# Optimization experiments

Hardware: AMD Instinct MI355X
Metric: run time of the kernel (lower is better)

The kernel has to match this reference:

```python
import jax, jax.numpy as jnp
import numpy as np

B, S, H, L, NH, DH, FF = 64, 128, 768, 6, 12, 64, 3072
VOCAB, MAXPOS, INTENT, TAGS = 30522, 512, 22, 122
LN_EPS = 1e-12
INV_SQRT_DH = float(1.0 / np.sqrt(DH))


def _ln(x, s, b):
    m = x.mean(-1, keepdims=True)
    v = ((x - m) ** 2).mean(-1, keepdims=True)
    return (x - m) * jax.lax.rsqrt(v + LN_EPS) * s + b


def setup_inputs():
    key = jax.random.key(0)
    cnt = [0]
    def nk():
        cnt[0] += 1
        return jax.random.fold_in(key, cnt[0])
    def nrm(shape):
        return (0.02 * jax.random.normal(nk(), shape)).astype(jnp.float32)
    inp = {
        'input_ids': jax.random.randint(nk(), (B, S), 0, VOCAB),
        'attention_mask': jnp.ones((B, S), jnp.int32),
        'intent_target': jax.random.randint(nk(), (B,), 0, INTENT),
        'slots_target': jax.random.randint(nk(), (B, S), 0, TAGS),
        'slots_mask': jnp.ones((B, S), jnp.int32),
        'word_emb': nrm((VOCAB, H)), 'pos_emb': nrm((MAXPOS, H)),
        'emb_ln_s': jnp.ones((H,)), 'emb_ln_b': jnp.zeros((H,)),
        'Wq': nrm((L, H, H)), 'bq': jnp.zeros((L, H)),
        'Wk': nrm((L, H, H)), 'bk': jnp.zeros((L, H)),
        'Wv': nrm((L, H, H)), 'bv': jnp.zeros((L, H)),
        'Wo': nrm((L, H, H)), 'bo': jnp.zeros((L, H)),
        'sa_ln_s': jnp.ones((L, H)), 'sa_ln_b': jnp.zeros((L, H)),
        'W1f': nrm((L, H, FF)), 'b1f': jnp.zeros((L, FF)),
        'W2f': nrm((L, FF, H)), 'b2f': jnp.zeros((L, H)),
        'out_ln_s': jnp.ones((L, H)), 'out_ln_b': jnp.zeros((L, H)),
        'iW1': nrm((H, 64)), 'ib1': jnp.zeros((64,)),
        'iW2': nrm((64, INTENT)), 'ib2': jnp.zeros((INTENT,)),
        'sW1': nrm((H, 256)), 'sb1': jnp.zeros((256,)),
        'sW2': nrm((256, TAGS)), 'sb2': jnp.zeros((TAGS,)),
        'crf_start': nrm((TAGS,)), 'crf_end': nrm((TAGS,)), 'crf_trans': nrm((TAGS, TAGS)),
        'log_vars': jnp.zeros((2,)),
    }
    return inp


def _encoder(input_ids, attention_mask, word_emb, pos_emb, emb_ln_s, emb_ln_b,
             Wq, bq, Wk, bk, Wv, bv, Wo, bo, sa_ln_s, sa_ln_b,
             W1f, b1f, W2f, b2f, out_ln_s, out_ln_b):
    x = word_emb[input_ids] + pos_emb[jnp.arange(S)][None]
    x = _ln(x, emb_ln_s, emb_ln_b)
    neg = jnp.where(attention_mask[:, None, None, :] > 0, 0.0, -1e9).astype(x.dtype)
    for i in range(L):
        q = (x @ Wq[i] + bq[i]).reshape(B, S, NH, DH).transpose(0, 2, 1, 3)
        k = (x @ Wk[i] + bk[i]).reshape(B, S, NH, DH).transpose(0, 2, 1, 3)
        v = (x @ Wv[i] + bv[i]).reshape(B, S, NH, DH).transpose(0, 2, 1, 3)
        scores = jnp.einsum('bhqd,bhkd->bhqk', q, k) * INV_SQRT_DH + neg
        attn = jax.nn.softmax(scores, -1)
        ctx = jnp.einsum('bhqk,bhkd->bhqd', attn, v).transpose(0, 2, 1, 3).reshape(B, S, H)
        x = _ln(x + ctx @ Wo[i] + bo[i], sa_ln_s[i], sa_ln_b[i])
        h = jax.nn.gelu(x @ W1f[i] + b1f[i], approximate=False) @ W2f[i] + b2f[i]
        x = _ln(x + h, out_ln_s[i], out_ln_b[i])
    return x


def _crf_llh(emis, tags, mask, crf_start, crf_end, crf_trans):
    # pytorch-crf log-likelihood, reduction='sum'. emis [B,S,T], mask bool [B,S]
    fmask = mask.astype(emis.dtype)
    emit_sc = jnp.take_along_axis(emis, tags[..., None], -1)[..., 0]          # [B,S]
    trans_sc = crf_trans[tags[:, :-1], tags[:, 1:]]                            # [B,S-1]
    last_idx = mask.sum(1) - 1
    last_tag = tags[jnp.arange(B), last_idx]
    num = (crf_start[tags[:, 0]] + emit_sc[:, 0]
           + ((trans_sc + emit_sc[:, 1:]) * fmask[:, 1:]).sum(1)
           + crf_end[last_tag])
    def fstep(alpha, xs):
        emit_t, m_t = xs
        nxt = jax.nn.logsumexp(alpha[:, :, None] + crf_trans[None] + emit_t[:, None, :], axis=1)
        return jnp.where(m_t[:, None], nxt, alpha), None
    alpha0 = crf_start[None] + emis[:, 0]
    alpha, _ = jax.lax.scan(fstep, alpha0, (emis[:, 1:].transpose(1, 0, 2), mask[:, 1:].T))
    denom = jax.nn.logsumexp(alpha + crf_end[None], -1)
    return jnp.sum(num - denom)


def _viterbi(emis, mask, crf_start, crf_end, crf_trans):
    ident = jnp.arange(TAGS)[None, :]
    def vstep(alpha, xs):
        emit_t, m_t = xs
        score = alpha[:, :, None] + crf_trans[None] + emit_t[:, None, :]      # [B,T,T]
        bp = jnp.where(m_t[:, None], jnp.argmax(score, 1), ident)
        alpha = jnp.where(m_t[:, None], jnp.max(score, 1), alpha)
        return alpha, bp
    alpha0 = crf_start[None] + emis[:, 0]
    alpha, bps = jax.lax.scan(vstep, alpha0, (emis[:, 1:].transpose(1, 0, 2), mask[:, 1:].T))
    last = jnp.argmax(alpha + crf_end[None], -1)                               # [B]
    def bstep(tag, bp):
        prev = jnp.take_along_axis(bp, tag[:, None], 1)[:, 0]
        return prev, prev
    _, prevs = jax.lax.scan(bstep, last, bps, reverse=True)                    # [S-1,B]
    return jnp.concatenate([prevs, last[None]], 0).T                           # [B,S]


def reference(input_ids, attention_mask, intent_target, slots_target, slots_mask,
              word_emb, pos_emb, emb_ln_s, emb_ln_b,
              Wq, bq, Wk, bk, Wv, bv, Wo, bo, sa_ln_s, sa_ln_b,
              W1f, b1f, W2f, b2f, out_ln_s, out_ln_b,
              iW1, ib1, iW2, ib2, sW1, sb1, sW2, sb2,
              crf_start, crf_end, crf_trans, log_vars):
    x = _encoder(input_ids, attention_mask, word_emb, pos_emb, emb_ln_s, emb_ln_b,
                 Wq, bq, Wk, bk, Wv, bv, Wo, bo, sa_ln_s, sa_ln_b,
                 W1f, b1f, W2f, b2f, out_ln_s, out_ln_b)
    # intent head: linear1(relu(cls)) -> relu -> linear2 (dropout = eval identity)
    intent_logits = jax.nn.relu(jax.nn.relu(x[:, 0]) @ iW1 + ib1) @ iW2 + ib2
    intent_loss = (jax.nn.logsumexp(intent_logits, -1)
                   - jnp.take_along_axis(intent_logits, intent_target[:, None], 1)[:, 0])
    intent_pred = jnp.argmax(intent_logits, -1)
    # slots head
    slots_logits = jax.nn.relu(jax.nn.relu(x) @ sW1 + sb1) @ sW2 + sb2
    mask = slots_mask.astype(bool)
    slots_loss = -_crf_llh(slots_logits, slots_target, mask, crf_start, crf_end, crf_trans)
    p1 = jnp.exp(-log_vars[0])
    p2 = jnp.exp(-log_vars[1])
    joint_loss = jnp.sum(p1 * intent_loss + log_vars[0]) + (p2 * slots_loss + log_vars[1])
    slots_pred = _viterbi(slots_logits, mask, crf_start, crf_end, crf_trans)
    return joint_loss, slots_pred, intent_pred
```

## Files before the change

### kernel.cpp

```cpp
#include <hip/hip_runtime.h>
#include <math.h>

#define B_      64
#define S_      128
#define H_      768
#define L_      6
#define NH_     12
#define DH_     64
#define FF_     3072
#define INTENT_ 22
#define TAGS_   122
#define NT_     (B_*S_)
#define LN_EPS  1e-12f
#define INV_SQRT_DH 0.125f

#define GF_RELU_IN  1
#define GF_RELU_OUT 2
#define GF_GELU_OUT 4
#define GF_ACCUM    8

typedef _Float16 half8 __attribute__((ext_vector_type(8)));
typedef float    f32x4 __attribute__((ext_vector_type(4)));

__device__ inline float block_reduce_sum256(float v, float* red) {
    int tid = threadIdx.x;
    red[tid] = v; __syncthreads();
    for (int off = 128; off > 0; off >>= 1) {
        if (tid < off) red[tid] += red[tid + off];
        __syncthreads();
    }
    float r = red[0]; __syncthreads();
    return r;
}

__global__ __launch_bounds__(256) void embed_ln_kernel(
    const int* __restrict__ ids, const float* __restrict__ we,
    const float* __restrict__ pe, const float* __restrict__ gs,
    const float* __restrict__ gb, float* __restrict__ X)
{
    __shared__ float red[256];
    int bs = blockIdx.x;
    int sq = bs % S_;
    int id = ids[bs];
    const float* wrow = we + (size_t)id * H_;
    const float* prow = pe + (size_t)sq * H_;
    float z[3];
    #pragma unroll
    for (int r = 0; r < 3; r++) {
        int h = threadIdx.x + 256*r;
        z[r] = wrow[h] + prow[h];
    }
    float sum = z[0] + z[1] + z[2];
    sum = block_reduce_sum256(sum, red);
    float m = sum * (1.0f / H_);
    float vs = 0.f;
    #pragma unroll
    for (int r = 0; r < 3; r++) { float d = z[r]-m; vs += d*d; }
    vs = block_reduce_sum256(vs, red) * (1.0f / H_);
    float rstd = 1.0f / sqrtf(vs + LN_EPS);
    float* out = X + (size_t)bs * H_;
    #pragma unroll
    for (int r = 0; r < 3; r++) {
        int h = threadIdx.x + 256*r;
        out[h] = (z[r]-m)*rstd*gs[h] + gb[h];
    }
}

__global__ __launch_bounds__(256) void residual_ln_kernel(
    float* __restrict__ X, const float* __restrict__ Y,
    const float* __restrict__ gs, const float* __restrict__ gb)
{
    __shared__ float red[256];
    int bs = blockIdx.x;
    float* xrow = X + (size_t)bs * H_;
    const float* yrow = Y + (size_t)bs * H_;
    float z[3];
    #pragma unroll
    for (int r = 0; r < 3; r++) {
        int h = threadIdx.x + 256*r;
        z[r] = xrow[h] + yrow[h];
    }
    float sum = z[0] + z[1] + z[2];
    sum = block_reduce_sum256(sum, red);
    float m = sum * (1.0f / H_);
    float vs = 0.f;
    #pragma unroll
    for (int r = 0; r < 3; r++) { float d = z[r]-m; vs += d*d; }
    vs = block_reduce_sum256(vs, red) * (1.0f / H_);
    float rstd = 1.0f / sqrtf(vs + LN_EPS);
    #pragma unroll
    for (int r = 0; r < 3; r++) {
        int h = threadIdx.x + 256*r;
        xrow[h] = (z[r]-m)*rstd*gs[h] + gb[h];
    }
}

__global__ __launch_bounds__(256) void wconv_kernel(
    const float* __restrict__ W0, const float* __restrict__ W1,
    const float* __restrict__ W2, int K, int N,
    _Float16* __restrict__ OH, _Float16* __restrict__ OL, long zoff)
{
    __shared__ float t[64][65];
    int z = blockIdx.z;
    const float* W = (z==0) ? W0 : ((z==1) ? W1 : W2);
    OH += (long)z*zoff; OL += (long)z*zoff;
    int k0 = blockIdx.x*64, n0 = blockIdx.y*64;
    int tid = threadIdx.x;
    int lr = tid>>4, lc = (tid&15)*4;
    #pragma unroll
    for (int p = 0; p < 4; p++) {
        float4 v = *(const float4*)&W[(size_t)(k0+lr+16*p)*N + n0 + lc];
        t[lr+16*p][lc]   = v.x; t[lr+16*p][lc+1] = v.y;
        t[lr+16*p][lc+2] = v.z; t[lr+16*p][lc+3] = v.w;
    }
    __syncthreads();
    int n = tid>>2, kb = (tid&3)*16;
    union U { _Float16 h[8]; uint4 u; } h0, h1, l0, l1;
    #pragma unroll
    for (int e = 0; e < 8; e++) {
        float x = t[kb+e][n];
        _Float16 hv = (_Float16)x;
        h0.h[e] = hv; l0.h[e] = (_Float16)(x - (float)hv);
    }
    #pragma unroll
    for (int e = 0; e < 8; e++) {
        float x = t[kb+8+e][n];
        _Float16 hv = (_Float16)x;
        h1.h[e] = hv; l1.h[e] = (_Float16)(x - (float)hv);
    }
    size_t ob = (size_t)(n0+n)*K + k0 + kb;
    *(uint4*)&OH[ob]   = h0.u;
    *(uint4*)&OH[ob+8] = h1.u;
    *(uint4*)&OL[ob]   = l0.u;
    *(uint4*)&OL[ob+8] = l1.u;
}

#define ASTR2 40
__global__ __launch_bounds__(256) void gemm2_kernel(
    const float* __restrict__ A32, const _Float16* __restrict__ AhG,
    const _Float16* __restrict__ AlG, int lda,
    const _Float16* __restrict__ WtH, const _Float16* __restrict__ WtL,
    int ldw, long wz,
    float* __restrict__ C, _Float16* __restrict__ OH, _Float16* __restrict__ OL,
    int ldc, long oz,
    const float* __restrict__ bias0, const float* __restrict__ bias1,
    const float* __restrict__ bias2,
    int M, int N, int K, int flags)
{
    __shared__ __align__(16) _Float16 Ah[128*ASTR2], Al[128*ASTR2];
    __shared__ __align__(16) _Float16 Bh[128*ASTR2], Bl[128*ASTR2];
    int z = blockIdx.z;
    WtH += (long)z*wz; WtL += (long)z*wz;
    if (OH) { OH += (long)z*oz; OL += (long)z*oz; }
    const float* bias = (z==0) ? bias0 : ((z==1) ? bias1 : bias2);
    const int tid = threadIdx.x, lane = tid&63, wid = tid>>6;
    const int wm = wid&1, wn = wid>>1;
    const int l15 = lane&15, quad = lane>>4;
    const int m0 = blockIdx.x*128, n0 = blockIdx.y*128;
    const int am = tid>>1, ak = (tid&1)*16;

    f32x4 acc[4][4];
    #pragma unroll
    for (int i = 0; i < 4; i++)
        #pragma unroll
        for (int j = 0; j < 4; j++)
            acc[i][j] = (f32x4){0.f,0.f,0.f,0.f};

    for (int k0 = 0; k0 < K; k0 += 32) {
        {
            const _Float16* bp = &WtH[(size_t)(n0+am)*ldw + k0 + ak];
            *(uint4*)&Bh[am*ASTR2 + ak]     = *(const uint4*)bp;
            *(uint4*)&Bh[am*ASTR2 + ak + 8] = *(const uint4*)(bp+8);
            const _Float16* bq2 = &WtL[(size_t)(n0+am)*ldw + k0 + ak];
            *(uint4*)&Bl[am*ASTR2 + ak]     = *(const uint4*)bq2;
            *(uint4*)&Bl[am*ASTR2 + ak + 8] = *(const uint4*)(bq2+8);
        }
        if (A32) {
            const float* ap = &A32[(size_t)(m0+am)*lda + k0 + ak];
            float vv[16];
            *(float4*)&vv[0]  = *(const float4*)ap;
            *(float4*)&vv[4]  = *(const float4*)(ap+4);
            *(float4*)&vv[8]  = *(const float4*)(ap+8);
            *(float4*)&vv[12] = *(const float4*)(ap+12);
            if (flags & GF_RELU_IN) {
                #pragma unroll
                for (int e = 0; e < 16; e++) vv[e] = fmaxf(vv[e], 0.f);
            }
            union U { _Float16 h[8]; uint4 u; } h0, h1, l0, l1;
            #pragma unroll
            for (int e = 0; e < 8; e++) {
                _Float16 hv = (_Float16)vv[e];
                h0.h[e] = hv; l0.h[e] = (_Float16)(vv[e] - (float)hv);
            }
            #pragma unroll
            for (int e = 0; e < 8; e++) {
                _Float16 hv = (_Float16)vv[8+e];
                h1.h[e] = hv; l1.h[e] = (_Float16)(vv[8+e] - (float)hv);
            }
            *(uint4*)&Ah[am*ASTR2 + ak]     = h0.u;
            *(uint4*)&Ah[am*ASTR2 + ak + 8] = h1.u;
            *(uint4*)&Al[am*ASTR2 + ak]     = l0.u;
            *(uint4*)&Al[am*ASTR2 + ak + 8] = l1.u;
        } else {
            const _Float16* ap = &AhG[(size_t)(m0+am)*lda + k0 + ak];
            *(uint4*)&Ah[am*ASTR2 + ak]     = *(const uint4*)ap;
            *(uint4*)&Ah[am*ASTR2 + ak + 8] = *(const uint4*)(ap+8);
            const _Float16* aq = &AlG[(size_t)(m0+am)*lda + k0 + ak];
            *(uint4*)&Al[am*ASTR2 + ak]     = *(const uint4*)aq;
            *(uint4*)&Al[am*ASTR2 + ak + 8] = *(const uint4*)(aq+8);
        }
        __syncthreads();
        half8 afh[4], afl[4], bfh[4], bfl[4];
        #pragma unroll
        for (int i = 0; i < 4; i++) {
            int m = wm*64 + i*16 + l15;
            afh[i] = *(const half8*)&Ah[m*ASTR2 + quad*8];
            afl[i] = *(const half8*)&Al[m*ASTR2 + quad*8];
            int n = wn*64 + i*16 + l15;
            bfh[i] = *(const half8*)&Bh[n*ASTR2 + quad*8];
            bfl[i] = *(const half8*)&Bl[n*ASTR2 + quad*8];
        }
        #pragma unroll
        for (int i = 0; i < 4; i++)
            #pragma unroll
            for (int j = 0; j < 4; j++) {
                acc[i][j] = __builtin_amdgcn_mfma_f32_16x16x32_f16(afh[i], bfh[j], acc[i][j], 0,0,0);
                acc[i][j] = __builtin_amdgcn_mfma_f32_16x16x32_f16(afh[i], bfl[j], acc[i][j], 0,0,0);
                acc[i][j] = __builtin_amdgcn_mfma_f32_16x16x32_f16(afl[i], bfh[j], acc[i][j], 0,0,0);
            }
        __syncthreads();
    }
    #pragma unroll
    for (int i = 0; i < 4; i++)
        #pragma unroll
        for (int j = 0; j < 4; j++)
            #pragma unroll
            for (int r = 0; r < 4; r++) {
                int gm = m0 + wm*64 + i*16 + quad*4 + r;
                int gn = n0 + wn*64 + j*16 + l15;
                float v = acc[i][j][r];
                if (bias) v += bias[gn];
                if (flags & GF_ACCUM) v += C[(size_t)gm*ldc + gn];
                if (flags & GF_RELU_OUT) v = fmaxf(v, 0.f);
                if (flags & GF_GELU_OUT) v = 0.5f*v*(1.0f + erff(v*0.70710678118654752f));
                if (OH) {
                    _Float16 hv = (_Float16)v;
                    OH[(size_t)gm*ldc + gn] = hv;
                    OL[(size_t)gm*ldc + gn] = (_Float16)(v - (float)hv);
                } else {
                    C[(size_t)gm*ldc + gn] = v;
                }
            }
}

#define BM 64
#define BN 64
#define BK 16
__global__ __launch_bounds__(256) void gemm_kernel(
    const float* __restrict__ A, int lda,
    const float* __restrict__ W, int ldb,
    float* __restrict__ C, int ldc,
    const float* __restrict__ bias,
    int M, int N, int K, int flags)
{
    __shared__ __align__(16) float As[BK][BM+4];
    __shared__ __align__(16) float Bs[BK][BN+4];
    int tid = threadIdx.x;
    int tx = tid & 15, ty = tid >> 4;
    int m0 = blockIdx.x * BM;
    int n0 = blockIdx.y * BN;
    float acc[4][4] = {};
    for (int k0 = 0; k0 < K; k0 += BK) {
        #pragma unroll
        for (int r = 0; r < 4; r++) {
            int li = tid + 256*r;
            int m  = li >> 4;
            int kk = li & 15;
            int gm = m0 + m, gk = k0 + kk;
            float v = (gm < M && gk < K) ? A[(size_t)gm*lda + gk] : 0.f;
            if (flags & GF_RELU_IN) v = fmaxf(v, 0.f);
            As[kk][m] = v;
        }
        #pragma unroll
        for (int r = 0; r < 4; r++) {
            int li = tid + 256*r;
            int kk = li >> 6;
            int n  = li & 63;
            int gk = k0 + kk, gn = n0 + n;
            Bs[kk][n] = (gk < K && gn < N) ? W[(size_t)gk*ldb + gn] : 0.f;
        }
        __syncthreads();
        #pragma unroll
        for (int kk = 0; kk < BK; kk++) {
            float4 a  = *(const float4*)&As[kk][ty*4];
            float4 bb = *(const float4*)&Bs[kk][tx*4];
            float av[4] = {a.x, a.y, a.z, a.w};
            float bv[4] = {bb.x, bb.y, bb.z, bb.w};
            #pragma unroll
            for (int i = 0; i < 4; i++)
                #pragma unroll
                for (int j = 0; j < 4; j++)
                    acc[i][j] += av[i] * bv[j];
        }
        __syncthreads();
    }
    #pragma unroll
    for (int i = 0; i < 4; i++) {
        int gm = m0 + ty*4 + i;
        if (gm >= M) continue;
        #pragma unroll
        for (int j = 0; j < 4; j++) {
            int gn = n0 + tx*4 + j;
            if (gn >= N) continue;
            float v = acc[i][j];
            if (bias) v += bias[gn];
            if (flags & GF_ACCUM) v += C[(size_t)gm*ldc + gn];
            if (flags & GF_RELU_OUT) v = fmaxf(v, 0.f);
            if (flags & GF_GELU_OUT) v = 0.5f*v*(1.0f + erff(v*0.70710678118654752f));
            C[(size_t)gm*ldc + gn] = v;
        }
    }
}

__device__ inline int scidx(int row, int col) {
    return row*128 + (((col>>2) ^ (row&7))<<2) + (col&3);
}
__global__ __launch_bounds__(256) void attn2_kernel(
    const _Float16* __restrict__ QhG, const _Float16* __restrict__ QlG,
    const _Float16* __restrict__ KhG, const _Float16* __restrict__ KlG,
    const _Float16* __restrict__ VhG, const _Float16* __restrict__ VlG,
    const int* __restrict__ amask,
    _Float16* __restrict__ Ch, _Float16* __restrict__ Cl)
{
    __shared__ __align__(16) char smem[65536];
    _Float16* Qh_s = (_Float16*)smem;
    _Float16* Ql_s = Qh_s + 64*72;
    _Float16* Kh_s = Ql_s + 64*72;
    _Float16* Kl_s = Kh_s + 128*72;
    float*    Sc   = (float*)smem;
    _Float16* Vth  = (_Float16*)(smem + 32768);
    _Float16* Vtl  = Vth + 64*128;

    int blk = blockIdx.x;
    int qh2 = blk & 1;
    int bh  = blk >> 1;
    int b = bh / NH_, hh = bh % NH_;
    const int tid = threadIdx.x, lane = tid&63, wid = tid>>6;
    const int l15 = lane&15, quad = lane>>4;
    const int qr = wid*16;
    size_t tokb = (size_t)b*S_*H_ + (size_t)hh*DH_;

    float nmask[8];
    #pragma unroll
    for (int j = 0; j < 8; j++)
        nmask[j] = (amask[b*S_ + j*16 + l15] > 0) ? 0.f : -1e9f;

    {
        int row = tid>>2, part = (tid&3)*16;
        size_t qg = tokb + (size_t)(qh2*64 + row)*H_ + part;
        *(uint4*)&Qh_s[row*72 + part] = *(const uint4*)(QhG + qg);
        *(uint4*)&Ql_s[row*72 + part] = *(const uint4*)(QlG + qg);
        #pragma unroll
        for (int p = 0; p < 2; p++) {
            int krow = row + p*64;
            size_t kg = tokb + (size_t)krow*H_ + part;
            *(uint4*)&Kh_s[krow*72 + part] = *(const uint4*)(KhG + kg);
            *(uint4*)&Kl_s[krow*72 + part] = *(const uint4*)(KlG + kg);
        }
    }
    __syncthreads();

    f32x4 acc1[8];
    #pragma unroll
    for (int j = 0; j < 8; j++) acc1[j] = (f32x4){0.f,0.f,0.f,0.f};
    half8 aqh[2], aql[2];
    #pragma unroll
    for (int kc = 0; kc < 2; kc++) {
        aqh[kc] = *(const half8*)&Qh_s[(qr + l15)*72 + kc*32 + quad*8];
        aql[kc] = *(const half8*)&Ql_s[(qr + l15)*72 + kc*32 + quad*8];
    }
    #pragma unroll
    for (int j = 0; j < 8; j++) {
        #pragma unroll
        for (int kc = 0; kc < 2; kc++) {
            half8 bkh = *(const half8*)&Kh_s[(j*16 + l15)*72 + kc*32 + quad*8];
            half8 bkl = *(const half8*)&Kl_s[(j*16 + l15)*72 + kc*32 + quad*8];
            acc1[j] = __builtin_amdgcn_mfma_f32_16x16x32_f16(aqh[kc], bkh, acc1[j], 0,0,0);
            acc1[j] = __builtin_amdgcn_mfma_f32_16x16x32_f16(aqh[kc], bkl, acc1[j], 0,0,0);
            acc1[j] = __builtin_amdgcn_mfma_f32_16x16x32_f16(aql[kc], bkh, acc1[j], 0,0,0);
        }
    }
    __syncthreads();

    #pragma unroll
    for (int j = 0; j < 8; j++)
        #pragma unroll
        for (int r = 0; r < 4; r++) {
            int row = qr + quad*4 + r;
            int col = j*16 + l15;
            Sc[scidx(row, col)] = acc1[j][r]*INV_SQRT_DH + nmask[j];
        }
    {
        int key = tid>>1, dh = (tid&1)*32;
        union V32 { _Float16 h[32]; uint4 u[4]; } bufh, bufl;
        #pragma unroll
        for (int e = 0; e < 4; e++) {
            bufh.u[e] = *(const uint4*)(VhG + tokb + (size_t)key*H_ + dh + e*8);
            bufl.u[e] = *(const uint4*)(VlG + tokb + (size_t)key*H_ + dh + e*8);
        }
        int kg = key>>3, kr = key&7;
        #pragma unroll
        for (int e = 0; e < 32; e++) {
            int d = dh + e;
            int pos = kg ^ (d & 7);
            Vth[d*128 + pos*8 + kr] = bufh.h[e];
            Vtl[d*128 + pos*8 + kr] = bufl.h[e];
        }
    }
    __syncthreads();

    {
        int row = tid>>2, part = (tid&3)*32;
        float mx = -INFINITY;
        #pragma unroll 8
        for (int e = 0; e < 32; e++)
            mx = fmaxf(mx, Sc[scidx(row, part+e)]);
        mx = fmaxf(mx, __shfl_xor(mx, 1));
        mx = fmaxf(mx, __shfl_xor(mx, 2));
        float s = 0.f;
        #pragma unroll 8
        for (int e = 0; e < 32; e++) {
            int idx = scidx(row, part+e);
            float ev = expf(Sc[idx] - mx);
            Sc[idx] = ev; s += ev;
        }
        s += __shfl_xor(s, 1);
        s += __shfl_xor(s, 2);
        float inv = 1.0f / s;
        #pragma unroll 8
        for (int e = 0; e < 32; e++)
            Sc[scidx(row, part+e)] *= inv;
    }
    __syncthreads();

    f32x4 acc2[4];
    #pragma unroll
    for (int jd = 0; jd < 4; jd++) acc2[jd] = (f32x4){0.f,0.f,0.f,0.f};
    #pragma unroll
    for (int kc = 0; kc < 4; kc++) {
        int q = qr + l15;
        int g16 = kc*8 + quad*2;
        float4 p0 = *(const float4*)&Sc[q*128 + ((g16   ^ (q&7))<<2)];
        float4 p1 = *(const float4*)&Sc[q*128 + (((g16+1) ^ (q&7))<<2)];
        float pv[8] = {p0.x,p0.y,p0.z,p0.w, p1.x,p1.y,p1.z,p1.w};
        union U { _Float16 h[8]; half8 v; } ph, pl;
        #pragma unroll
        for (int e = 0; e < 8; e++) {
            _Float16 hv = (_Float16)pv[e];
            ph.h[e] = hv; pl.h[e] = (_Float16)(pv[e] - (float)hv);
        }
        #pragma unroll
        for (int jd = 0; jd < 4; jd++) {
            int n = jd*16 + l15;
            int pos = (kc*4 + quad) ^ (n & 7);
            half8 vh = *(const half8*)&Vth[n*128 + pos*8];
            half8 vl = *(const half8*)&Vtl[n*128 + pos*8];
            acc2[jd] = __builtin_amdgcn_mfma_f32_16x16x32_f16(ph.v, vh, acc2[jd], 0,0,0);
            acc2[jd] = __builtin_amdgcn_mfma_f32_16x16x32_f16(ph.v, vl, acc2[jd], 0,0,0);
            acc2[jd] = __builtin_amdgcn_mfma_f32_16x16x32_f16(pl.v, vh, acc2[jd], 0,0,0);
        }
    }
    #pragma unroll
    for (int jd = 0; jd < 4; jd++)
        #pragma unroll
        for (int r = 0; r < 4; r++) {
            int row = qr + quad*4 + r;
            int token = b*S_ + qh2*64 + row;
            int d = jd*16 + l15;
            float v = acc2[jd][r];
            _Float16 hv = (_Float16)v;
            Ch[(size_t)token*H_ + hh*DH_ + d] = hv;
            Cl[(size_t)token*H_ + hh*DH_ + d] = (_Float16)(v - (float)hv);
        }
}

__global__ __launch_bounds__(64) void intent_kernel(
    const float* __restrict__ X, const float* __restrict__ iW1,
    const float* __restrict__ ib1, const float* __restrict__ iW2,
    const float* __restrict__ ib2, const int* __restrict__ tgt,
    float* __restrict__ iloss, float* __restrict__ outf)
{
    int b = blockIdx.x; int j = threadIdx.x;
    __shared__ float h1[64];
    __shared__ float lg[32];
    const float* x0 = X + (size_t)b*S_*H_;
    float acc = ib1[j];
    for (int h = 0; h < H_; h++) acc += fmaxf(x0[h], 0.f) * iW1[(size_t)h*64 + j];
    h1[j] = fmaxf(acc, 0.f);
    __syncthreads();
    if (j < INTENT_) {
        float l = ib2[j];
        for (int k = 0; k < 64; k++) l += h1[k]*iW2[k*INTENT_ + j];
        lg[j] = l;
    }
    __syncthreads();
    if (j == 0) {
        float mx = -INFINITY; int bi = 0;
        for (int c = 0; c < INTENT_; c++) if (lg[c] > mx) { mx = lg[c]; bi = c; }
        float sm = 0.f;
        for (int c = 0; c < INTENT_; c++) sm += expf(lg[c]-mx);
        float lse = mx + logf(sm);
        iloss[b] = lse - lg[tgt[b]];
        outf[1 + (size_t)NT_ + b] = (float)bi;
    }
}

#define TSTR 124
__global__ __launch_bounds__(128) void crf_llh_kernel(
    const float* __restrict__ E_, const int* __restrict__ tags,
    const int* __restrict__ mask, const float* __restrict__ start,
    const float* __restrict__ endv, const float* __restrict__ trans,
    float* __restrict__ crfv)
{
    int b = blockIdx.x; int j = threadIdx.x;
    __shared__ __align__(16) float etT[TAGS_*TSTR];
    __shared__ __align__(16) float alpha[TAGS_];
    __shared__ __align__(16) float ealpha[TAGS_];
    __shared__ __align__(16) float red[128];
    const float* E = E_ + (size_t)b*S_*TAGS_;
    for (int i = 0; i < TAGS_; i++)
        if (j < TAGS_) etT[(size_t)j*TSTR + i] = expf(trans[i*TAGS_ + j]);
    if (j < TAGS_) alpha[j] = start[j] + E[j];
    __syncthreads();

    for (int t = 1; t < S_; t++) {
        float av = (j < TAGS_) ? alpha[j] : -1e30f;
        red[j] = av; __syncthreads();
        for (int off = 64; off > 0; off >>= 1) {
            if (j < off) red[j] = fmaxf(red[j], red[j+off]);
            __syncthreads();
        }
        float mx = red[0];
        if (j < TAGS_) ealpha[j] = expf(av - mx);
        __syncthreads();
        float nv = 0.f;
        int m_t = mask[b*S_ + t];
        if (j < TAGS_) {
            const float* tr = &etT[(size_t)j*TSTR];
            float s = 0.f;
            #pragma unroll 5
            for (int i = 0; i < 120; i += 4) {
                float4 ea = *(const float4*)&ealpha[i];
                float4 tt = *(const float4*)&tr[i];
                s += ea.x*tt.x + ea.y*tt.y + ea.z*tt.z + ea.w*tt.w;
            }
            s += ealpha[120]*tr[120] + ealpha[121]*tr[121];
            nv = mx + logf(s) + E[t*TAGS_ + j];
        }
        __syncthreads();
        if (j < TAGS_ && m_t) alpha[j] = nv;
        __syncthreads();
    }

    int tg  = (j < S_) ? tags[b*S_ + j] : 0;
    int mk  = (j < S_) ? mask[b*S_ + j] : 0;
    int tgp = (j >= 1 && j < S_) ? tags[b*S_ + j - 1] : 0;
    float term = 0.f;
    if (j >= 1 && j < S_ && mk)
        term = trans[tgp*TAGS_ + tg] + E[(size_t)j*TAGS_ + tg];
    red[j] = term; __syncthreads();
    for (int off = 64; off > 0; off >>= 1) {
        if (j < off) red[j] += red[j+off];
        __syncthreads();
    }
    float numsum = red[0]; __syncthreads();
    red[j] = (float)mk; __syncthreads();
    for (int off = 64; off > 0; off >>= 1) {
        if (j < off) red[j] += red[j+off];
        __syncthreads();
    }
    int msum = (int)red[0]; __syncthreads();
    float dv = (j < TAGS_) ? alpha[j] + endv[j] : -1e30f;
    red[j] = dv; __syncthreads();
    for (int off = 64; off > 0; off >>= 1) {
        if (j < off) red[j] = fmaxf(red[j], red[j+off]);
        __syncthreads();
    }
    float dmx = red[0]; __syncthreads();
    red[j] = (j < TAGS_) ? expf(dv - dmx) : 0.f;
    __syncthreads();
    for (int off = 64; off > 0; off >>= 1) {
        if (j < off) red[j] += red[j+off];
        __syncthreads();
    }
    if (j == 0) {
        float denom = dmx + logf(red[0]);
        int tag0 = tags[b*S_];
        int last_tag = tags[b*S_ + (msum - 1)];
        float num = start[tag0] + E[tag0] + numsum + endv[last_tag];
        crfv[b] = num - denom;
    }
}

__global__ __launch_bounds__(128) void viterbi_kernel(
    const float* __restrict__ E_, const int* __restrict__ mask,
    const float* __restrict__ start, const float* __restrict__ endv,
    const float* __restrict__ trans, int* __restrict__ BP,
    float* __restrict__ outf)
{
    int b = blockIdx.x; int j = threadIdx.x;
    __shared__ __align__(16) float tT[TAGS_*TSTR];
    __shared__ __align__(16) float alpha[TAGS_];
    const float* E = E_ + (size_t)b*S_*TAGS_;
    for (int i = 0; i < TAGS_; i++)
        if (j < TAGS_) tT[(size_t)j*TSTR + i] = trans[i*TAGS_ + j];
    if (j < TAGS_) alpha[j] = start[j] + E[j];
    __syncthreads();
    for (int t = 1; t < S_; t++) {
        int m_t = mask[b*S_ + t];
        float nv = 0.f; int nb = 0;
        if (j < TAGS_) {
            const float* tr = &tT[(size_t)j*TSTR];
            float best = -1e30f; int bi = 0;
            #pragma unroll 5
            for (int i = 0; i < 120; i += 4) {
                float4 al = *(const float4*)&alpha[i];
                float4 tt = *(const float4*)&tr[i];
                float v0 = al.x + tt.x; if (v0 > best) { best = v0; bi = i;   }
                float v1 = al.y + tt.y; if (v1 > best) { best = v1; bi = i+1; }
                float v2 = al.z + tt.z; if (v2 > best) { best = v2; bi = i+2; }
                float v3 = al.w + tt.w; if (v3 > best) { best = v3; bi = i+3; }
            }
            { float v = alpha[120] + tr[120]; if (v > best) { best = v; bi = 120; } }
            { float v = alpha[121] + tr[121]; if (v > best) { best = v; bi = 121; } }
            if (m_t) { nv = best + E[(size_t)t*TAGS_ + j]; nb = bi; }
            else     { nv = alpha[j];                       nb = j;  }
        }
        __syncthreads();
        if (j < TAGS_) {
            alpha[j] = nv;
            BP[((size_t)b*(S_-1) + (t-1))*TAGS_ + j] = nb;
        }
        __syncthreads();
    }
    if (j == 0) {
        float best = -1e30f; int bi = 0;
        for (int i = 0; i < TAGS_; i++) {
            float v = alpha[i] + endv[i];
            if (v > best) { best = v; bi = i; }
        }
        int tag = bi;
        outf[1 + (size_t)b*S_ + (S_-1)] = (float)tag;
        for (int t = S_-1; t >= 1; t--) {
            tag = BP[((size_t)b*(S_-1) + (t-1))*TAGS_ + tag];
            outf[1 + (size_t)b*S_ + (t-1)] = (float)tag;
        }
    }
}

__global__ void combine_kernel(const float* __restrict__ iloss,
                               const float* __restrict__ crfv,
                               const float* __restrict__ lv,
                               float* __restrict__ outf)
{
    if (threadIdx.x == 0 && blockIdx.x == 0) {
        float si = 0.f, sc = 0.f;
        for (int b = 0; b < B_; b++) { si += iloss[b]; sc += crfv[b]; }
        float p1 = expf(-lv[0]), p2 = expf(-lv[1]);
        float slots_loss = -sc;
        outf[0] = p1*si + (float)B_*lv[0] + p2*slots_loss + lv[1];
    }
}

extern "C" void kernel_launch(void* const* d_in, const int* in_sizes, int n_in,
                              void* d_out, int out_size, void* d_ws, size_t ws_size,
                              hipStream_t stream) {
    const int*   ids   = (const int*)  d_in[0];
    const int*   amask = (const int*)  d_in[1];
    const int*   itgt  = (const int*)  d_in[2];
    const int*   stgt  = (const int*)  d_in[3];
    const int*   smask = (const int*)  d_in[4];
    const float* we    = (const float*)d_in[5];
    const float* pe    = (const float*)d_in[6];
    const float* embs  = (const float*)d_in[7];
    const float* embb  = (const float*)d_in[8];
    const float* Wq    = (const float*)d_in[9];
    const float* bq    = (const float*)d_in[10];
    const float* Wk    = (const float*)d_in[11];
    const float* bk    = (const float*)d_in[12];
    const float* Wv    = (const float*)d_in[13];
    const float* bv    = (const float*)d_in[14];
    const float* Wo    = (const float*)d_in[15];
    const float* bo    = (const float*)d_in[16];
    const float* sas   = (const float*)d_in[17];
    const float* sab   = (const float*)d_in[18];
    const float* W1f   = (const float*)d_in[19];
    const float* b1f   = (const float*)d_in[20];
    const float* W2f   = (const float*)d_in[21];
    const float* b2f   = (const float*)d_in[22];
    const float* ols   = (const float*)d_in[23];
    const float* olb   = (const float*)d_in[24];
    const float* iW1   = (const float*)d_in[25];
    const float* ib1   = (const float*)d_in[26];
    const float* iW2   = (const float*)d_in[27];
    const float* ib2   = (const float*)d_in[28];
    const float* sW1   = (const float*)d_in[29];
    const float* sb1   = (const float*)d_in[30];
    const float* sW2   = (const float*)d_in[31];
    const float* sb2   = (const float*)d_in[32];
    const float* crfs  = (const float*)d_in[33];
    const float* crfe  = (const float*)d_in[34];
    const float* crft  = (const float*)d_in[35];
    const float* lv    = (const float*)d_in[36];

    float* outf = (float*)d_out;
    float* wsf  = (float*)d_ws;
    const long NBf = (long)NT_ * H_;
    const long NTH = NBf;
    const long HH  = (long)H_ * H_;
    const long WCAP = 2359296;

    float*     X   = wsf;
    _Float16*  qh  = (_Float16*)(wsf + NBf);
    _Float16 *Qh = qh,        *Ql = qh + NTH,
             *Kh = qh + 2*NTH,*Kl = qh + 3*NTH,
             *Vh = qh + 4*NTH,*Vl = qh + 5*NTH;
    _Float16 *Fh = qh, *Fl = qh + (long)NT_*1536;
    float*     H1     = (float*)(wsf + NBf);
    float*     logits = H1 + (long)NT_*256;
    int*       BP     = (int*)(logits + (long)NT_*122);
    _Float16*  Ch  = (_Float16*)(wsf + 4*NBf);
    _Float16*  Cl  = Ch + NTH;
    float*     Yb  = wsf + 5*NBf;
    _Float16*  WAh = (_Float16*)(wsf + 6*NBf);
    _Float16*  WBh = (_Float16*)(wsf + 6*NBf + WCAP);
    float*     iloss = wsf + 6*NBf + 2*WCAP;
    float*     crfv  = iloss + 64;

    auto wconv = [&](const float* w0, const float* w1, const float* w2,
                     int K, int N, _Float16* oh, _Float16* ol, long zoff, int nz) {
        dim3 g(K/64, N/64, nz);
        hipLaunchKernelGGL(wconv_kernel, g, dim3(256), 0, stream,
                           w0, w1, w2, K, N, oh, ol, zoff);
    };
    auto g2 = [&](const float* A32, const _Float16* AhG, const _Float16* AlG, int lda,
                  const _Float16* WtH, const _Float16* WtL, int ldw, long wz,
                  float* C, _Float16* OH, _Float16* OL, int ldc, long oz,
                  const float* b0, const float* b1, const float* b2,
                  int M, int N, int K, int flags, int nz) {
        dim3 g(M/128, N/128, nz);
        hipLaunchKernelGGL(gemm2_kernel, g, dim3(256), 0, stream,
                           A32, AhG, AlG, lda, WtH, WtL, ldw, wz,
                           C, OH, OL, ldc, oz, b0, b1, b2, M, N, K, flags);
    };

    hipLaunchKernelGGL(embed_ln_kernel, dim3(NT_), dim3(256), 0, stream,
                       ids, we, pe, embs, embb, X);

    for (int i = 0; i < L_; i++) {
        const long WO = (long)i*HH;
        wconv(Wq + WO, Wk + WO, Wv + WO, H_, H_, WAh, WAh + 3*HH, HH, 3);
        g2(X, nullptr, nullptr, H_, WAh, WAh + 3*HH, H_, HH,
           nullptr, Qh, Ql, H_, 2*NTH,
           bq + i*H_, bk + i*H_, bv + i*H_, NT_, H_, H_, 0, 3);
        hipLaunchKernelGGL(attn2_kernel, dim3(B_*NH_*2), dim3(256), 0, stream,
                           Qh, Ql, Kh, Kl, Vh, Vl, amask, Ch, Cl);
        wconv(Wo + WO, Wo + WO, Wo + WO, H_, H_, WBh, WBh + HH, 0, 1);
        g2(nullptr, Ch, Cl, H_, WBh, WBh + HH, H_, 0,
           Yb, nullptr, nullptr, H_, 0,
           bo + i*H_, nullptr, nullptr, NT_, H_, H_, 0, 1);
        hipLaunchKernelGGL(residual_ln_kernel, dim3(NT_), dim3(256), 0, stream,
                           X, Yb, sas + i*H_, sab + i*H_);
        wconv(W1f + (long)i*H_*FF_, nullptr, nullptr, H_, FF_, WAh, WAh + WCAP, 0, 1);
        wconv(W2f + (long)i*FF_*H_, nullptr, nullptr, FF_, H_, WBh, WBh + WCAP, 0, 1);
        for (int c = 0; c < 2; c++) {
            const int CW = FF_/2;
            g2(X, nullptr, nullptr, H_,
               WAh + (long)c*CW*H_, WAh + WCAP + (long)c*CW*H_, H_, 0,
               nullptr, Fh, Fl, CW, 0,
               b1f + (long)i*FF_ + c*CW, nullptr, nullptr,
               NT_, CW, H_, GF_GELU_OUT, 1);
            g2(nullptr, Fh, Fl, CW,
               WBh + (long)c*CW, WBh + WCAP + (long)c*CW, FF_, 0,
               Yb, nullptr, nullptr, H_, 0,
               (c == 0) ? (b2f + i*H_) : nullptr, nullptr, nullptr,
               NT_, H_, CW, (c == 0) ? 0 : GF_ACCUM, 1);
        }
        hipLaunchKernelGGL(residual_ln_kernel, dim3(NT_), dim3(256), 0, stream,
                           X, Yb, ols + i*H_, olb + i*H_);
    }

    hipLaunchKernelGGL(intent_kernel, dim3(B_), dim3(64), 0, stream,
                       X, iW1, ib1, iW2, ib2, itgt, iloss, outf);

    wconv(sW1, nullptr, nullptr, H_, 256, WAh, WAh + (long)256*H_, 0, 1);
    g2(X, nullptr, nullptr, H_, WAh, WAh + (long)256*H_, H_, 0,
       H1, nullptr, nullptr, 256, 0,
       sb1, nullptr, nullptr, NT_, 256, H_, GF_RELU_IN | GF_RELU_OUT, 1);
    {
        dim3 g((NT_+BM-1)/BM, (TAGS_+BN-1)/BN);
        hipLaunchKernelGGL(gemm_kernel, g, dim3(256), 0, stream,
                           H1, 256, sW2, TAGS_, logits, TAGS_, sb2,
                           NT_, TAGS_, 256, 0);
    }

    hipLaunchKernelGGL(crf_llh_kernel, dim3(B_), dim3(128), 0, stream,
                       logits, stgt, smask, crfs, crfe, crft, crfv);
    hipLaunchKernelGGL(viterbi_kernel, dim3(B_), dim3(128), 0, stream,
                       logits, smask, crfs, crfe, crft, BP, outf);

    hipLaunchKernelGGL(combine_kernel, dim3(1), dim3(64), 0, stream,
                       iloss, crfv, lv, outf);
}
```

Measured before the change: 4.904 ms.

## Keep activations as fp16 hi/lo pairs, fuse residuals into GEMMs, async LDS loads

Activations now stay in split fp16 hi/lo form throughout the encoder, so the GEMM no longer converts fp32 A tiles per k-step. The residual add moves into the GEMM epilogue and a lighter LN kernel reads the result. Tiles are loaded with global_load_lds direct-to-LDS copies without padding, one wave per operand. Wq/Wk/Wv/Wo are converted in a single launch, and the CRF likelihood and Viterbi passes are merged into one kernel. The unpadded LDS layout may add bank conflicts, and accumulating the residual in fp16 pairs may cost some precision.

```diff
diff --git a/kernel.cpp b/kernel.cpp
--- a/kernel.cpp
+++ b/kernel.cpp
@@ -1,5 +1,6 @@
 #include <hip/hip_runtime.h>
 #include <math.h>
+#include <stdint.h>
 
 #define B_      64
 #define S_      128
@@ -14,95 +15,137 @@
 #define LN_EPS  1e-12f
 #define INV_SQRT_DH 0.125f
 
-#define GF_RELU_IN  1
 #define GF_RELU_OUT 2
 #define GF_GELU_OUT 4
-#define GF_ACCUM    8
+#define GF_ADDRES   16
+#define GF_ACCH     32
 
 typedef _Float16 half8 __attribute__((ext_vector_type(8)));
 typedef float    f32x4 __attribute__((ext_vector_type(4)));
 
-__device__ inline float block_reduce_sum256(float v, float* red) {
-    int tid = threadIdx.x;
-    red[tid] = v; __syncthreads();
-    for (int off = 128; off > 0; off >>= 1) {
-        if (tid < off) red[tid] += red[tid + off];
-        __syncthreads();
-    }
-    float r = red[0]; __syncthreads();
-    return r;
+__device__ __forceinline__ void gld16(const _Float16* g, _Float16* l) {
+    __builtin_amdgcn_global_load_lds(
+        (const __attribute__((address_space(1))) unsigned int*)(uintptr_t)g,
+        (__attribute__((address_space(3))) unsigned int*)(unsigned int)(uintptr_t)l,
+        16, 0, 0);
+}
+
+__device__ inline float wave_max(float v){
+    #pragma unroll
+    for (int d = 32; d; d >>= 1) v = fmaxf(v, __shfl_xor(v, d));
+    return v;
+}
+__device__ inline float wave_sum(float v){
+    #pragma unroll
+    for (int d = 32; d; d >>= 1) v += __shfl_xor(v, d);
+    return v;
 }
 
 __global__ __launch_bounds__(256) void embed_ln_kernel(
     const int* __restrict__ ids, const float* __restrict__ we,
     const float* __restrict__ pe, const float* __restrict__ gs,
-    const float* __restrict__ gb, float* __restrict__ X)
+    const float* __restrict__ gb, _Float16* __restrict__ Xh,
+    _Float16* __restrict__ Xl)
 {
     __shared__ float red[256];
     int bs = blockIdx.x;
     int sq = bs % S_;
     int id = ids[bs];
+    int tid = threadIdx.x;
     const float* wrow = we + (size_t)id * H_;
     const float* prow = pe + (size_t)sq * H_;
     float z[3];
     #pragma unroll
     for (int r = 0; r < 3; r++) {
-        int h = threadIdx.x + 256*r;
+        int h = tid + 256*r;
         z[r] = wrow[h] + prow[h];
     }
-    float sum = z[0] + z[1] + z[2];
-    sum = block_reduce_sum256(sum, red);
-    float m = sum * (1.0f / H_);
+    float sum = z[0]+z[1]+z[2];
+    red[tid] = sum; __syncthreads();
+    for (int off = 128; off > 0; off >>= 1) {
+        if (tid < off) red[tid] += red[tid+off];
+        __syncthreads();
+    }
+    float m = red[0] * (1.0f/H_); __syncthreads();
     float vs = 0.f;
     #pragma unroll
     for (int r = 0; r < 3; r++) { float d = z[r]-m; vs += d*d; }
-    vs = block_reduce_sum256(vs, red) * (1.0f / H_);
-    float rstd = 1.0f / sqrtf(vs + LN_EPS);
-    float* out = X + (size_t)bs * H_;
+    red[tid] = vs; __syncthreads();
+    for (int off = 128; off > 0; off >>= 1) {
+        if (tid < off) red[tid] += red[tid+off];
+        __syncthreads();
+    }
+    float rstd = 1.0f / sqrtf(red[0]*(1.0f/H_) + LN_EPS);
     #pragma unroll
     for (int r = 0; r < 3; r++) {
-        int h = threadIdx.x + 256*r;
-        out[h] = (z[r]-m)*rstd*gs[h] + gb[h];
-    }
-}
-
-__global__ __launch_bounds__(256) void residual_ln_kernel(
-    float* __restrict__ X, const float* __restrict__ Y,
-    const float* __restrict__ gs, const float* __restrict__ gb)
+        int h = tid + 256*r;
+        float val = (z[r]-m)*rstd*gs[h] + gb[h];
+        _Float16 hv = (_Float16)val;
+        Xh[(size_t)bs*H_ + h] = hv;
+        Xl[(size_t)bs*H_ + h] = (_Float16)(val - (float)hv);
+    }
+}
+
+__global__ __launch_bounds__(384) void ln2_kernel(
+    const _Float16* __restrict__ Sh, const _Float16* __restrict__ Sl,
+    const float* __restrict__ gs, const float* __restrict__ gb,
+    _Float16* __restrict__ Xh, _Float16* __restrict__ Xl,
+    _Float16* __restrict__ Rh, _Float16* __restrict__ Rl)
 {
-    __shared__ float red[256];
-    int bs = blockIdx.x;
-    float* xrow = X + (size_t)bs * H_;
-    const float* yrow = Y + (size_t)bs * H_;
-    float z[3];
-    #pragma unroll
-    for (int r = 0; r < 3; r++) {
-        int h = threadIdx.x + 256*r;
-        z[r] = xrow[h] + yrow[h];
-    }
-    float sum = z[0] + z[1] + z[2];
-    sum = block_reduce_sum256(sum, red);
-    float m = sum * (1.0f / H_);
-    float vs = 0.f;
-    #pragma unroll
-    for (int r = 0; r < 3; r++) { float d = z[r]-m; vs += d*d; }
-    vs = block_reduce_sum256(vs, red) * (1.0f / H_);
-    float rstd = 1.0f / sqrtf(vs + LN_EPS);
-    #pragma unroll
-    for (int r = 0; r < 3; r++) {
-        int h = threadIdx.x + 256*r;
-        xrow[h] = (z[r]-m)*rstd*gs[h] + gb[h];
+    __shared__ float red[512];
+    int bs = blockIdx.x, tid = threadIdx.x;
+    size_t base = (size_t)bs*H_ + tid*2;
+    union UU { _Float16 h[2]; unsigned u; };
+    UU uh, ul;
+    uh.u = *(const unsigned*)(Sh + base);
+    ul.u = *(const unsigned*)(Sl + base);
+    float z0 = (float)uh.h[0] + (float)ul.h[0];
+    float z1 = (float)uh.h[1] + (float)ul.h[1];
+    red[tid] = z0 + z1;
+    if (tid < 128) red[384+tid] = 0.f;
+    __syncthreads();
+    for (int off = 256; off > 0; off >>= 1) {
+        if (tid < off) red[tid] += red[tid+off];
+        __syncthreads();
+    }
+    float m = red[0] * (1.0f/H_);
+    __syncthreads();
+    float d0 = z0-m, d1 = z1-m;
+    red[tid] = d0*d0 + d1*d1;
+    if (tid < 128) red[384+tid] = 0.f;
+    __syncthreads();
+    for (int off = 256; off > 0; off >>= 1) {
+        if (tid < off) red[tid] += red[tid+off];
+        __syncthreads();
+    }
+    float rstd = 1.0f / sqrtf(red[0]*(1.0f/H_) + LN_EPS);
+    float2 gv = *(const float2*)(gs + tid*2);
+    float2 bv = *(const float2*)(gb + tid*2);
+    float v0 = d0*rstd*gv.x + bv.x;
+    float v1 = d1*rstd*gv.y + bv.y;
+    UU oh, ol;
+    oh.h[0] = (_Float16)v0; ol.h[0] = (_Float16)(v0 - (float)oh.h[0]);
+    oh.h[1] = (_Float16)v1; ol.h[1] = (_Float16)(v1 - (float)oh.h[1]);
+    *(unsigned*)(Xh + base) = oh.u;
+    *(unsigned*)(Xl + base) = ol.u;
+    if (Rh) {
+        float r0 = fmaxf(v0, 0.f), r1 = fmaxf(v1, 0.f);
+        UU rh, rl;
+        rh.h[0] = (_Float16)r0; rl.h[0] = (_Float16)(r0 - (float)rh.h[0]);
+        rh.h[1] = (_Float16)r1; rl.h[1] = (_Float16)(r1 - (float)rh.h[1]);
+        *(unsigned*)(Rh + base) = rh.u;
+        *(unsigned*)(Rl + base) = rl.u;
     }
 }
 
 __global__ __launch_bounds__(256) void wconv_kernel(
     const float* __restrict__ W0, const float* __restrict__ W1,
-    const float* __restrict__ W2, int K, int N,
-    _Float16* __restrict__ OH, _Float16* __restrict__ OL, long zoff)
+    const float* __restrict__ W2, const float* __restrict__ W3,
+    int K, int N, _Float16* __restrict__ OH, _Float16* __restrict__ OL, long zoff)
 {
     __shared__ float t[64][65];
     int z = blockIdx.z;
-    const float* W = (z==0) ? W0 : ((z==1) ? W1 : W2);
+    const float* W = (z==0) ? W0 : ((z==1) ? W1 : ((z==2) ? W2 : W3));
     OH += (long)z*zoff; OL += (long)z*zoff;
     int k0 = blockIdx.x*64, n0 = blockIdx.y*64;
     int tid = threadIdx.x;
@@ -135,29 +178,36 @@
     *(uint4*)&OL[ob+8] = l1.u;
 }
 
-#define ASTR2 40
-__global__ __launch_bounds__(256) void gemm2_kernel(
-    const float* __restrict__ A32, const _Float16* __restrict__ AhG,
-    const _Float16* __restrict__ AlG, int lda,
-    const _Float16* __restrict__ WtH, const _Float16* __restrict__ WtL,
+__global__ __launch_bounds__(256) void gemm3_kernel(
+    const _Float16* __restrict__ AhG, const _Float16* __restrict__ AlG, int lda,
+    const _Float16* __restrict__ WtHb, const _Float16* __restrict__ WtLb,
     int ldw, long wz,
-    float* __restrict__ C, _Float16* __restrict__ OH, _Float16* __restrict__ OL,
+    float* __restrict__ C, _Float16* __restrict__ OHb, _Float16* __restrict__ OLb,
     int ldc, long oz,
+    const _Float16* __restrict__ Rh, const _Float16* __restrict__ Rl, int ldr,
     const float* __restrict__ bias0, const float* __restrict__ bias1,
     const float* __restrict__ bias2,
-    int M, int N, int K, int flags)
+    int K, int flags)
 {
-    __shared__ __align__(16) _Float16 Ah[128*ASTR2], Al[128*ASTR2];
-    __shared__ __align__(16) _Float16 Bh[128*ASTR2], Bl[128*ASTR2];
-    int z = blockIdx.z;
-    WtH += (long)z*wz; WtL += (long)z*wz;
-    if (OH) { OH += (long)z*oz; OL += (long)z*oz; }
+    __shared__ __align__(16) _Float16 Ah[128*32], Al[128*32];
+    __shared__ __align__(16) _Float16 Bh[128*32], Bl[128*32];
+    const int z = blockIdx.z;
+    const _Float16* WtH = WtHb + (long)z*wz;
+    const _Float16* WtL = WtLb + (long)z*wz;
+    _Float16* oh = OHb ? OHb + (long)z*oz : (_Float16*)0;
+    _Float16* ol = OLb ? OLb + (long)z*oz : (_Float16*)0;
     const float* bias = (z==0) ? bias0 : ((z==1) ? bias1 : bias2);
     const int tid = threadIdx.x, lane = tid&63, wid = tid>>6;
     const int wm = wid&1, wn = wid>>1;
     const int l15 = lane&15, quad = lane>>4;
     const int m0 = blockIdx.x*128, n0 = blockIdx.y*128;
-    const int am = tid>>1, ak = (tid&1)*16;
+
+    const _Float16* gsrc; _Float16* lbuf; int ld_s; int r0;
+    if (wid == 0)      { gsrc = AhG; lbuf = Ah; ld_s = lda; r0 = m0; }
+    else if (wid == 1) { gsrc = AlG; lbuf = Al; ld_s = lda; r0 = m0; }
+    else if (wid == 2) { gsrc = WtH; lbuf = Bh; ld_s = ldw; r0 = n0; }
+    else               { gsrc = WtL; lbuf = Bl; ld_s = ldw; r0 = n0; }
+    const _Float16* gbase = gsrc + (size_t)(r0 + (lane>>2))*ld_s + (lane&3)*8;
 
     f32x4 acc[4][4];
     #pragma unroll
@@ -167,58 +217,19 @@
             acc[i][j] = (f32x4){0.f,0.f,0.f,0.f};
 
     for (int k0 = 0; k0 < K; k0 += 32) {
-        {
-            const _Float16* bp = &WtH[(size_t)(n0+am)*ldw + k0 + ak];
-            *(uint4*)&Bh[am*ASTR2 + ak]     = *(const uint4*)bp;
-            *(uint4*)&Bh[am*ASTR2 + ak + 8] = *(const uint4*)(bp+8);
-            const _Float16* bq2 = &WtL[(size_t)(n0+am)*ldw + k0 + ak];
-            *(uint4*)&Bl[am*ASTR2 + ak]     = *(const uint4*)bq2;
-            *(uint4*)&Bl[am*ASTR2 + ak + 8] = *(const uint4*)(bq2+8);
-        }
-        if (A32) {
-            const float* ap = &A32[(size_t)(m0+am)*lda + k0 + ak];
-            float vv[16];
-            *(float4*)&vv[0]  = *(const float4*)ap;
-            *(float4*)&vv[4]  = *(const float4*)(ap+4);
-            *(float4*)&vv[8]  = *(const float4*)(ap+8);
-            *(float4*)&vv[12] = *(const float4*)(ap+12);
-            if (flags & GF_RELU_IN) {
-                #pragma unroll
-                for (int e = 0; e < 16; e++) vv[e] = fmaxf(vv[e], 0.f);
-            }
-            union U { _Float16 h[8]; uint4 u; } h0, h1, l0, l1;
-            #pragma unroll
-            for (int e = 0; e < 8; e++) {
-                _Float16 hv = (_Float16)vv[e];
-                h0.h[e] = hv; l0.h[e] = (_Float16)(vv[e] - (float)hv);
-            }
-            #pragma unroll
-            for (int e = 0; e < 8; e++) {
-                _Float16 hv = (_Float16)vv[8+e];
-                h1.h[e] = hv; l1.h[e] = (_Float16)(vv[8+e] - (float)hv);
-            }
-            *(uint4*)&Ah[am*ASTR2 + ak]     = h0.u;
-            *(uint4*)&Ah[am*ASTR2 + ak + 8] = h1.u;
-            *(uint4*)&Al[am*ASTR2 + ak]     = l0.u;
-            *(uint4*)&Al[am*ASTR2 + ak + 8] = l1.u;
-        } else {
-            const _Float16* ap = &AhG[(size_t)(m0+am)*lda + k0 + ak];
-            *(uint4*)&Ah[am*ASTR2 + ak]     = *(const uint4*)ap;
-            *(uint4*)&Ah[am*ASTR2 + ak + 8] = *(const uint4*)(ap+8);
-            const _Float16* aq = &AlG[(size_t)(m0+am)*lda + k0 + ak];
-            *(uint4*)&Al[am*ASTR2 + ak]     = *(const uint4*)aq;
-            *(uint4*)&Al[am*ASTR2 + ak + 8] = *(const uint4*)(aq+8);
-        }
+        #pragma unroll
+        for (int q = 0; q < 8; q++)
+            gld16(gbase + (size_t)(q*16)*ld_s + k0, lbuf + q*512);
         __syncthreads();
         half8 afh[4], afl[4], bfh[4], bfl[4];
         #pragma unroll
         for (int i = 0; i < 4; i++) {
             int m = wm*64 + i*16 + l15;
-            afh[i] = *(const half8*)&Ah[m*ASTR2 + quad*8];
-            afl[i] = *(const half8*)&Al[m*ASTR2 + quad*8];
+            afh[i] = *(const half8*)&Ah[m*32 + quad*8];
+            afl[i] = *(const half8*)&Al[m*32 + quad*8];
             int n = wn*64 + i*16 + l15;
-            bfh[i] = *(const half8*)&Bh[n*ASTR2 + quad*8];
-            bfl[i] = *(const half8*)&Bl[n*ASTR2 + quad*8];
+            bfh[i] = *(const half8*)&Bh[n*32 + quad*8];
+            bfl[i] = *(const half8*)&Bl[n*32 + quad*8];
         }
         #pragma unroll
         for (int i = 0; i < 4; i++)
@@ -240,15 +251,21 @@
                 int gn = n0 + wn*64 + j*16 + l15;
                 float v = acc[i][j][r];
                 if (bias) v += bias[gn];
-                if (flags & GF_ACCUM) v += C[(size_t)gm*ldc + gn];
+                size_t ox = (size_t)gm*ldc + gn;
+                if (flags & GF_ADDRES) {
+                    size_t rx = (size_t)gm*ldr + gn;
+                    v += (float)Rh[rx] + (float)Rl[rx];
+                }
+                if (flags & GF_ACCH)
+                    v += (float)oh[ox] + (float)ol[ox];
                 if (flags & GF_RELU_OUT) v = fmaxf(v, 0.f);
                 if (flags & GF_GELU_OUT) v = 0.5f*v*(1.0f + erff(v*0.70710678118654752f));
-                if (OH) {
+                if (oh) {
                     _Float16 hv = (_Float16)v;
-                    OH[(size_t)gm*ldc + gn] = hv;
-                    OL[(size_t)gm*ldc + gn] = (_Float16)(v - (float)hv);
+                    oh[ox] = hv;
+                    ol[ox] = (_Float16)(v - (float)hv);
                 } else {
-                    C[(size_t)gm*ldc + gn] = v;
+                    C[ox] = v;
                 }
             }
 }
@@ -261,7 +278,7 @@
     const float* __restrict__ W, int ldb,
     float* __restrict__ C, int ldc,
     const float* __restrict__ bias,
-    int M, int N, int K, int flags)
+    int M, int N, int K)
 {
     __shared__ __align__(16) float As[BK][BM+4];
     __shared__ __align__(16) float Bs[BK][BN+4];
@@ -277,9 +294,7 @@
             int m  = li >> 4;
             int kk = li & 15;
             int gm = m0 + m, gk = k0 + kk;
-            float v = (gm < M && gk < K) ? A[(size_t)gm*lda + gk] : 0.f;
-            if (flags & GF_RELU_IN) v = fmaxf(v, 0.f);
-            As[kk][m] = v;
+            As[kk][m] = (gm < M && gk < K) ? A[(size_t)gm*lda + gk] : 0.f;
         }
         #pragma unroll
         for (int r = 0; r < 4; r++) {
@@ -314,9 +329,6 @@
             if (gn >= N) continue;
             float v = acc[i][j];
             if (bias) v += bias[gn];
-            if (flags & GF_ACCUM) v += C[(size_t)gm*ldc + gn];
-            if (flags & GF_RELU_OUT) v = fmaxf(v, 0.f);
-            if (flags & GF_GELU_OUT) v = 0.5f*v*(1.0f + erff(v*0.70710678118654752f));
             C[(size_t)gm*ldc + gn] = v;
         }
     }
@@ -485,7 +497,8 @@
 }
 
 __global__ __launch_bounds__(64) void intent_kernel(
-    const float* __restrict__ X, const float* __restrict__ iW1,
+    const _Float16* __restrict__ Xh, const _Float16* __restrict__ Xl,
+    const float* __restrict__ iW1,
     const float* __restrict__ ib1, const float* __restrict__ iW2,
     const float* __restrict__ ib2, const int* __restrict__ tgt,
     float* __restrict__ iloss, float* __restrict__ outf)
@@ -493,9 +506,13 @@
     int b = blockIdx.x; int j = threadIdx.x;
     __shared__ float h1[64];
     __shared__ float lg[32];
-    const float* x0 = X + (size_t)b*S_*H_;
+    const _Float16* x0h = Xh + (size_t)b*S_*H_;
+    const _Float16* x0l = Xl + (size_t)b*S_*H_;
     float acc = ib1[j];
-    for (int h = 0; h < H_; h++) acc += fmaxf(x0[h], 0.f) * iW1[(size_t)h*64 + j];
+    for (int h = 0; h < H_; h++) {
+        float x = (float)x0h[h] + (float)x0l[h];
+        acc += fmaxf(x, 0.f) * iW1[(size_t)h*64 + j];
+    }
     h1[j] = fmaxf(acc, 0.f);
     __syncthreads();
     if (j < INTENT_) {
@@ -515,145 +532,150 @@
     }
 }
 
-#define TSTR 124
-__global__ __launch_bounds__(128) void crf_llh_kernel(
+#define VST 130
+__global__ __launch_bounds__(512) void crf_vit_kernel(
     const float* __restrict__ E_, const int* __restrict__ tags,
     const int* __restrict__ mask, const float* __restrict__ start,
     const float* __restrict__ endv, const float* __restrict__ trans,
-    float* __restrict__ crfv)
-{
-    int b = blockIdx.x; int j = threadIdx.x;
-    __shared__ __align__(16) float etT[TAGS_*TSTR];
-    __shared__ __align__(16) float alpha[TAGS_];
-    __shared__ __align__(16) float ealpha[TAGS_];
-    __shared__ __align__(16) float red[128];
-    const float* E = E_ + (size_t)b*S_*TAGS_;
-    for (int i = 0; i < TAGS_; i++)
-        if (j < TAGS_) etT[(size_t)j*TSTR + i] = expf(trans[i*TAGS_ + j]);
-    if (j < TAGS_) alpha[j] = start[j] + E[j];
-    __syncthreads();
-
-    for (int t = 1; t < S_; t++) {
-        float av = (j < TAGS_) ? alpha[j] : -1e30f;
-        red[j] = av; __syncthreads();
-        for (int off = 64; off > 0; off >>= 1) {
-            if (j < off) red[j] = fmaxf(red[j], red[j+off]);
-            __syncthreads();
-        }
-        float mx = red[0];
-        if (j < TAGS_) ealpha[j] = expf(av - mx);
-        __syncthreads();
-        float nv = 0.f;
-        int m_t = mask[b*S_ + t];
-        if (j < TAGS_) {
-            const float* tr = &etT[(size_t)j*TSTR];
-            float s = 0.f;
-            #pragma unroll 5
-            for (int i = 0; i < 120; i += 4) {
-                float4 ea = *(const float4*)&ealpha[i];
-                float4 tt = *(const float4*)&tr[i];
-                s += ea.x*tt.x + ea.y*tt.y + ea.z*tt.z + ea.w*tt.w;
-            }
-            s += ealpha[120]*tr[120] + ealpha[121]*tr[121];
-            nv = mx + logf(s) + E[t*TAGS_ + j];
-        }
-        __syncthreads();
-        if (j < TAGS_ && m_t) alpha[j] = nv;
-        __syncthreads();
-    }
-
-    int tg  = (j < S_) ? tags[b*S_ + j] : 0;
-    int mk  = (j < S_) ? mask[b*S_ + j] : 0;
-    int tgp = (j >= 1 && j < S_) ? tags[b*S_ + j - 1] : 0;
-    float term = 0.f;
-    if (j >= 1 && j < S_ && mk)
-        term = trans[tgp*TAGS_ + tg] + E[(size_t)j*TAGS_ + tg];
-    red[j] = term; __syncthreads();
-    for (int off = 64; off > 0; off >>= 1) {
-        if (j < off) red[j] += red[j+off];
-        __syncthreads();
-    }
-    float numsum = red[0]; __syncthreads();
-    red[j] = (float)mk; __syncthreads();
-    for (int off = 64; off > 0; off >>= 1) {
-        if (j < off) red[j] += red[j+off];
-        __syncthreads();
-    }
-    int msum = (int)red[0]; __syncthreads();
-    float dv = (j < TAGS_) ? alpha[j] + endv[j] : -1e30f;
-    red[j] = dv; __syncthreads();
-    for (int off = 64; off > 0; off >>= 1) {
-        if (j < off) red[j] = fmaxf(red[j], red[j+off]);
-        __syncthreads();
-    }
-    float dmx = red[0]; __syncthreads();
-    red[j] = (j < TAGS_) ? expf(dv - dmx) : 0.f;
-    __syncthreads();
-    for (int off = 64; off > 0; off >>= 1) {
-        if (j < off) red[j] += red[j+off];
-        __syncthreads();
-    }
-    if (j == 0) {
-        float denom = dmx + logf(red[0]);
-        int tag0 = tags[b*S_];
-        int last_tag = tags[b*S_ + (msum - 1)];
-        float num = start[tag0] + E[tag0] + numsum + endv[last_tag];
-        crfv[b] = num - denom;
-    }
-}
-
-__global__ __launch_bounds__(128) void viterbi_kernel(
-    const float* __restrict__ E_, const int* __restrict__ mask,
-    const float* __restrict__ start, const float* __restrict__ endv,
-    const float* __restrict__ trans, int* __restrict__ BP,
+    float* __restrict__ crfv, unsigned char* __restrict__ BPg,
     float* __restrict__ outf)
 {
-    int b = blockIdx.x; int j = threadIdx.x;
-    __shared__ __align__(16) float tT[TAGS_*TSTR];
-    __shared__ __align__(16) float alpha[TAGS_];
+    __shared__ __align__(16) float tT[TAGS_*VST];
+    __shared__ float alpha[TAGS_+2];
+    __shared__ float ealpha[TAGS_+2];
+    __shared__ float mxbuf[16];
+    __shared__ int lastt;
+    int b = blockIdx.x;
+    int mode = blockIdx.y;
+    int tid = threadIdx.x, lane = tid&63, wid = tid>>6;
+    int j = tid>>2, p = tid&3;
+    int cnt = (p < 2) ? 31 : 30;
     const float* E = E_ + (size_t)b*S_*TAGS_;
-    for (int i = 0; i < TAGS_; i++)
-        if (j < TAGS_) tT[(size_t)j*TSTR + i] = trans[i*TAGS_ + j];
-    if (j < TAGS_) alpha[j] = start[j] + E[j];
-    __syncthreads();
-    for (int t = 1; t < S_; t++) {
-        int m_t = mask[b*S_ + t];
-        float nv = 0.f; int nb = 0;
-        if (j < TAGS_) {
-            const float* tr = &tT[(size_t)j*TSTR];
-            float best = -1e30f; int bi = 0;
-            #pragma unroll 5
-            for (int i = 0; i < 120; i += 4) {
-                float4 al = *(const float4*)&alpha[i];
-                float4 tt = *(const float4*)&tr[i];
-                float v0 = al.x + tt.x; if (v0 > best) { best = v0; bi = i;   }
-                float v1 = al.y + tt.y; if (v1 > best) { best = v1; bi = i+1; }
-                float v2 = al.z + tt.z; if (v2 > best) { best = v2; bi = i+2; }
-                float v3 = al.w + tt.w; if (v3 > best) { best = v3; bi = i+3; }
-            }
-            { float v = alpha[120] + tr[120]; if (v > best) { best = v; bi = 120; } }
-            { float v = alpha[121] + tr[121]; if (v > best) { best = v; bi = 121; } }
-            if (m_t) { nv = best + E[(size_t)t*TAGS_ + j]; nb = bi; }
-            else     { nv = alpha[j];                       nb = j;  }
-        }
-        __syncthreads();
-        if (j < TAGS_) {
-            alpha[j] = nv;
-            BP[((size_t)b*(S_-1) + (t-1))*TAGS_ + j] = nb;
-        }
-        __syncthreads();
-    }
-    if (j == 0) {
-        float best = -1e30f; int bi = 0;
-        for (int i = 0; i < TAGS_; i++) {
-            float v = alpha[i] + endv[i];
-            if (v > best) { best = v; bi = i; }
-        }
-        int tag = bi;
-        outf[1 + (size_t)b*S_ + (S_-1)] = (float)tag;
-        for (int t = S_-1; t >= 1; t--) {
-            tag = BP[((size_t)b*(S_-1) + (t-1))*TAGS_ + tag];
-            outf[1 + (size_t)b*S_ + (t-1)] = (float)tag;
+
+    if (j < TAGS_) {
+        for (int e = 0; e < cnt; e++) {
+            int i = 4*e + p;
+            float tv = trans[i*TAGS_ + j];
+            tT[j*VST + i] = mode ? tv : expf(tv);
+        }
+        if (p == 0) alpha[j] = start[j] + E[j];
+    }
+    __syncthreads();
+
+    if (mode == 0) {
+        for (int t = 1; t < S_; t++) {
+            if (wid == 0) {
+                float a = (lane < TAGS_) ? alpha[lane] : -3e38f;
+                if (lane + 64 < TAGS_) a = fmaxf(a, alpha[lane+64]);
+                a = wave_max(a);
+                if (lane == 0) mxbuf[0] = a;
+            }
+            __syncthreads();
+            float mx = mxbuf[0];
+            if (p == 0 && j < TAGS_) ealpha[j] = expf(alpha[j] - mx);
+            __syncthreads();
+            float s = 0.f;
+            if (j < TAGS_) {
+                const float* tr = &tT[j*VST];
+                for (int e = 0; e < cnt; e++) {
+                    int i = 4*e + p;
+                    s += ealpha[i]*tr[i];
+                }
+            }
+            s += __shfl_xor(s, 1);
+            s += __shfl_xor(s, 2);
+            int m_t = mask[b*S_ + t];
+            float ee = (j < TAGS_) ? E[(size_t)t*TAGS_ + j] : 0.f;
+            float nv = mx + logf(s) + ee;
+            __syncthreads();
+            if (p == 0 && j < TAGS_ && m_t) alpha[j] = nv;
+            __syncthreads();
+        }
+        float term = 0.f, mkf = 0.f;
+        if (tid < S_) {
+            int mk = mask[b*S_ + tid]; mkf = (float)mk;
+            if (tid >= 1 && mk) {
+                int tg = tags[b*S_ + tid], tgp = tags[b*S_ + tid - 1];
+                term = trans[tgp*TAGS_ + tg] + E[(size_t)tid*TAGS_ + tg];
+            }
+        }
+        if (wid < 2) {
+            float ts = wave_sum(term);
+            float ms = wave_sum(mkf);
+            if (lane == 0) { mxbuf[2+wid] = ts; mxbuf[4+wid] = ms; }
+        }
+        __syncthreads();
+        if (wid == 0) {
+            float v1 = (lane < TAGS_) ? alpha[lane] + endv[lane] : -3e38f;
+            float v2 = (lane+64 < TAGS_) ? alpha[lane+64] + endv[lane+64] : -3e38f;
+            float m = wave_max(fmaxf(v1, v2));
+            float sd = ((lane < TAGS_) ? expf(v1 - m) : 0.f)
+                     + ((lane+64 < TAGS_) ? expf(v2 - m) : 0.f);
+            sd = wave_sum(sd);
+            if (lane == 0) {
+                float denom = m + logf(sd);
+                float numsum = mxbuf[2] + mxbuf[3];
+                int msum = (int)(mxbuf[4] + mxbuf[5]);
+                int tag0 = tags[b*S_];
+                int last_tag = tags[b*S_ + (msum - 1)];
+                float num = start[tag0] + E[tag0] + numsum + endv[last_tag];
+                crfv[b] = num - denom;
+            }
+        }
+    } else {
+        size_t bpb = (size_t)b*(S_-1)*TAGS_;
+        for (int t = 1; t < S_; t++) {
+            float best = -3e38f; int bi = 0;
+            if (j < TAGS_) {
+                const float* tr = &tT[j*VST];
+                for (int e = 0; e < cnt; e++) {
+                    int i = 4*e + p;
+                    float v = alpha[i] + tr[i];
+                    if (v > best) { best = v; bi = i; }
+                }
+            }
+            {
+                float ov = __shfl_xor(best, 1); int oi = __shfl_xor(bi, 1);
+                if (ov > best || (ov == best && oi < bi)) { best = ov; bi = oi; }
+                ov = __shfl_xor(best, 2); oi = __shfl_xor(bi, 2);
+                if (ov > best || (ov == best && oi < bi)) { best = ov; bi = oi; }
+            }
+            int m_t = mask[b*S_ + t];
+            float ee = (j < TAGS_) ? E[(size_t)t*TAGS_ + j] : 0.f;
+            float nv; int nb;
+            if (m_t) { nv = best + ee; nb = bi; }
+            else     { nv = (j < TAGS_) ? alpha[j] : 0.f; nb = j; }
+            __syncthreads();
+            if (p == 0 && j < TAGS_) {
+                alpha[j] = nv;
+                BPg[bpb + (size_t)(t-1)*TAGS_ + j] = (unsigned char)nb;
+            }
+            __syncthreads();
+        }
+        if (wid == 0) {
+            float v; int idx;
+            float v1 = (lane < TAGS_) ? alpha[lane] + endv[lane] : -3e38f;
+            float v2 = (lane+64 < TAGS_) ? alpha[lane+64] + endv[lane+64] : -3e38f;
+            if (v2 > v1) { v = v2; idx = lane+64; } else { v = v1; idx = lane; }
+            #pragma unroll
+            for (int d = 32; d; d >>= 1) {
+                float ov = __shfl_xor(v, d); int oi = __shfl_xor(idx, d);
+                if (ov > v || (ov == v && oi < idx)) { v = ov; idx = oi; }
+            }
+            if (lane == 0) lastt = idx;
+        }
+        __syncthreads();
+        unsigned char* bpl = (unsigned char*)tT;
+        for (int o = tid; o < (S_-1)*TAGS_; o += 512)
+            bpl[o] = BPg[bpb + o];
+        __syncthreads();
+        if (tid == 0) {
+            int tag = lastt;
+            outf[1 + (size_t)b*S_ + (S_-1)] = (float)tag;
+            for (int t = S_-1; t >= 1; t--) {
+                tag = bpl[(t-1)*TAGS_ + tag];
+                outf[1 + (size_t)b*S_ + (t-1)] = (float)tag;
+            }
         }
     }
 }
@@ -715,99 +737,104 @@
 
     float* outf = (float*)d_out;
     float* wsf  = (float*)d_ws;
-    const long NBf = (long)NT_ * H_;
-    const long NTH = NBf;
-    const long HH  = (long)H_ * H_;
-    const long WCAP = 2359296;
-
-    float*     X   = wsf;
-    _Float16*  qh  = (_Float16*)(wsf + NBf);
-    _Float16 *Qh = qh,        *Ql = qh + NTH,
-             *Kh = qh + 2*NTH,*Kl = qh + 3*NTH,
-             *Vh = qh + 4*NTH,*Vl = qh + 5*NTH;
-    _Float16 *Fh = qh, *Fl = qh + (long)NT_*1536;
-    float*     H1     = (float*)(wsf + NBf);
-    float*     logits = H1 + (long)NT_*256;
-    int*       BP     = (int*)(logits + (long)NT_*122);
-    _Float16*  Ch  = (_Float16*)(wsf + 4*NBf);
-    _Float16*  Cl  = Ch + NTH;
-    float*     Yb  = wsf + 5*NBf;
-    _Float16*  WAh = (_Float16*)(wsf + 6*NBf);
-    _Float16*  WBh = (_Float16*)(wsf + 6*NBf + WCAP);
-    float*     iloss = wsf + 6*NBf + 2*WCAP;
-    float*     crfv  = iloss + 64;
-
-    auto wconv = [&](const float* w0, const float* w1, const float* w2,
-                     int K, int N, _Float16* oh, _Float16* ol, long zoff, int nz) {
-        dim3 g(K/64, N/64, nz);
-        hipLaunchKernelGGL(wconv_kernel, g, dim3(256), 0, stream,
-                           w0, w1, w2, K, N, oh, ol, zoff);
-    };
-    auto g2 = [&](const float* A32, const _Float16* AhG, const _Float16* AlG, int lda,
+    const long NTHh = (long)NT_ * H_;
+    const long NBf  = NTHh;
+    const long HH   = (long)H_ * H_;
+
+    _Float16* Xh = (_Float16*)wsf;
+    _Float16* Xl = Xh + NTHh;
+    float*    Pf = wsf + NBf;
+    _Float16* Ph = (_Float16*)Pf;
+    _Float16 *Qh = Ph, *Ql = Ph + NTHh, *Kh = Ph + 2*NTHh, *Kl = Ph + 3*NTHh,
+             *Vh = Ph + 4*NTHh, *Vl = Ph + 5*NTHh;
+    _Float16 *Sh = Ph, *Sl = Ph + NTHh;
+    _Float16* Fh = (_Float16*)(wsf + 2*NBf);
+    _Float16* Fl = (_Float16*)(wsf + 3*NBf);
+    _Float16* Ch = (_Float16*)(wsf + 4*NBf);
+    _Float16* Cl = Ch + NTHh;
+    const long wa0 = 5*NBf;
+    _Float16* WAh = (_Float16*)(wsf + wa0);
+    _Float16* WAl = WAh + 4*HH;
+    const long wb1 = wa0 + 2359296;
+    _Float16* WB1h = (_Float16*)(wsf + wb1);
+    _Float16* WB1l = WB1h + 2359296;
+    const long wb2 = wb1 + 2359296;
+    _Float16* WB2h = (_Float16*)(wsf + wb2);
+    _Float16* WB2l = WB2h + 2359296;
+    float* iloss = wsf + wb2 + 2359296;
+    float* crfv  = iloss + 64;
+    float* H1 = Pf;
+    float* logits = Pf + 2097152;
+    unsigned char* BPg = (unsigned char*)(Pf + 2097152 + 999424);
+
+    auto g3 = [&](int gy, int gz,
+                  const _Float16* A_h, const _Float16* A_l, int lda,
                   const _Float16* WtH, const _Float16* WtL, int ldw, long wz,
                   float* C, _Float16* OH, _Float16* OL, int ldc, long oz,
-                  const float* b0, const float* b1, const float* b2,
-                  int M, int N, int K, int flags, int nz) {
-        dim3 g(M/128, N/128, nz);
-        hipLaunchKernelGGL(gemm2_kernel, g, dim3(256), 0, stream,
-                           A32, AhG, AlG, lda, WtH, WtL, ldw, wz,
-                           C, OH, OL, ldc, oz, b0, b1, b2, M, N, K, flags);
+                  const _Float16* Rh, const _Float16* Rl,
+                  const float* b0, const float* b1_, const float* b2_,
+                  int K, int flags) {
+        hipLaunchKernelGGL(gemm3_kernel, dim3(NT_/128, gy, gz), dim3(256), 0, stream,
+                           A_h, A_l, lda, WtH, WtL, ldw, wz,
+                           C, OH, OL, ldc, oz, Rh, Rl, H_, b0, b1_, b2_, K, flags);
     };
 
     hipLaunchKernelGGL(embed_ln_kernel, dim3(NT_), dim3(256), 0, stream,
-                       ids, we, pe, embs, embb, X);
+                       ids, we, pe, embs, embb, Xh, Xl);
 
     for (int i = 0; i < L_; i++) {
         const long WO = (long)i*HH;
-        wconv(Wq + WO, Wk + WO, Wv + WO, H_, H_, WAh, WAh + 3*HH, HH, 3);
-        g2(X, nullptr, nullptr, H_, WAh, WAh + 3*HH, H_, HH,
-           nullptr, Qh, Ql, H_, 2*NTH,
-           bq + i*H_, bk + i*H_, bv + i*H_, NT_, H_, H_, 0, 3);
+        hipLaunchKernelGGL(wconv_kernel, dim3(12,12,4), dim3(256), 0, stream,
+                           Wq+WO, Wk+WO, Wv+WO, Wo+WO, H_, H_, WAh, WAl, HH);
+        g3(6, 3, Xh, Xl, H_, WAh, WAl, H_, HH,
+           nullptr, Ph, Ph+NTHh, H_, 2*NTHh, nullptr, nullptr,
+           bq+i*H_, bk+i*H_, bv+i*H_, H_, 0);
         hipLaunchKernelGGL(attn2_kernel, dim3(B_*NH_*2), dim3(256), 0, stream,
                            Qh, Ql, Kh, Kl, Vh, Vl, amask, Ch, Cl);
-        wconv(Wo + WO, Wo + WO, Wo + WO, H_, H_, WBh, WBh + HH, 0, 1);
-        g2(nullptr, Ch, Cl, H_, WBh, WBh + HH, H_, 0,
-           Yb, nullptr, nullptr, H_, 0,
-           bo + i*H_, nullptr, nullptr, NT_, H_, H_, 0, 1);
-        hipLaunchKernelGGL(residual_ln_kernel, dim3(NT_), dim3(256), 0, stream,
-                           X, Yb, sas + i*H_, sab + i*H_);
-        wconv(W1f + (long)i*H_*FF_, nullptr, nullptr, H_, FF_, WAh, WAh + WCAP, 0, 1);
-        wconv(W2f + (long)i*FF_*H_, nullptr, nullptr, FF_, H_, WBh, WBh + WCAP, 0, 1);
+        g3(6, 1, Ch, Cl, H_, WAh+3*HH, WAl+3*HH, H_, 0,
+           nullptr, Sh, Sl, H_, 0, Xh, Xl,
+           bo+i*H_, nullptr, nullptr, H_, GF_ADDRES);
+        hipLaunchKernelGGL(ln2_kernel, dim3(NT_), dim3(384), 0, stream,
+                           Sh, Sl, sas+i*H_, sab+i*H_, Xh, Xl,
+                           (_Float16*)nullptr, (_Float16*)nullptr);
+        hipLaunchKernelGGL(wconv_kernel, dim3(12,48,1), dim3(256), 0, stream,
+                           W1f+(long)i*H_*FF_, nullptr, nullptr, nullptr,
+                           H_, FF_, WB1h, WB1l, 0);
+        hipLaunchKernelGGL(wconv_kernel, dim3(48,12,1), dim3(256), 0, stream,
+                           W2f+(long)i*FF_*H_, nullptr, nullptr, nullptr,
+                           FF_, H_, WB2h, WB2l, 0);
         for (int c = 0; c < 2; c++) {
             const int CW = FF_/2;
-            g2(X, nullptr, nullptr, H_,
-               WAh + (long)c*CW*H_, WAh + WCAP + (long)c*CW*H_, H_, 0,
-               nullptr, Fh, Fl, CW, 0,
-               b1f + (long)i*FF_ + c*CW, nullptr, nullptr,
-               NT_, CW, H_, GF_GELU_OUT, 1);
-            g2(nullptr, Fh, Fl, CW,
-               WBh + (long)c*CW, WBh + WCAP + (long)c*CW, FF_, 0,
-               Yb, nullptr, nullptr, H_, 0,
-               (c == 0) ? (b2f + i*H_) : nullptr, nullptr, nullptr,
-               NT_, H_, CW, (c == 0) ? 0 : GF_ACCUM, 1);
-        }
-        hipLaunchKernelGGL(residual_ln_kernel, dim3(NT_), dim3(256), 0, stream,
-                           X, Yb, ols + i*H_, olb + i*H_);
+            g3(12, 1, Xh, Xl, H_,
+               WB1h+(long)c*CW*H_, WB1l+(long)c*CW*H_, H_, 0,
+               nullptr, Fh, Fl, CW, 0, nullptr, nullptr,
+               b1f+(long)i*FF_+c*CW, nullptr, nullptr, H_, GF_GELU_OUT);
+            g3(6, 1, Fh, Fl, CW,
+               WB2h+(long)c*CW, WB2l+(long)c*CW, FF_, 0,
+               nullptr, Sh, Sl, H_, 0, Xh, Xl,
+               (c==0) ? (b2f+i*H_) : nullptr, nullptr, nullptr,
+               CW, (c==0) ? GF_ADDRES : GF_ACCH);
+        }
+        hipLaunchKernelGGL(ln2_kernel, dim3(NT_), dim3(384), 0, stream,
+                           Sh, Sl, ols+i*H_, olb+i*H_, Xh, Xl,
+                           (i==L_-1) ? Ch : (_Float16*)nullptr,
+                           (i==L_-1) ? Cl : (_Float16*)nullptr);
     }
 
     hipLaunchKernelGGL(intent_kernel, dim3(B_), dim3(64), 0, stream,
-                       X, iW1, ib1, iW2, ib2, itgt, iloss, outf);
-
-    wconv(sW1, nullptr, nullptr, H_, 256, WAh, WAh + (long)256*H_, 0, 1);
-    g2(X, nullptr, nullptr, H_, WAh, WAh + (long)256*H_, H_, 0,
-       H1, nullptr, nullptr, 256, 0,
-       sb1, nullptr, nullptr, NT_, 256, H_, GF_RELU_IN | GF_RELU_OUT, 1);
-    {
-        dim3 g((NT_+BM-1)/BM, (TAGS_+BN-1)/BN);
-        hipLaunchKernelGGL(gemm_kernel, g, dim3(256), 0, stream,
-                           H1, 256, sW2, TAGS_, logits, TAGS_, sb2,
-                           NT_, TAGS_, 256, 0);
-    }
-
-    hipLaunchKernelGGL(crf_llh_kernel, dim3(B_), dim3(128), 0, stream,
-                       logits, stgt, smask, crfs, crfe, crft, crfv);
-    hipLaunchKernelGGL(viterbi_kernel, dim3(B_), dim3(128), 0, stream,
-                       logits, smask, crfs, crfe, crft, BP, outf);
+                       Xh, Xl, iW1, ib1, iW2, ib2, itgt, iloss, outf);
+
+    hipLaunchKernelGGL(wconv_kernel, dim3(12,4,1), dim3(256), 0, stream,
+                       sW1, nullptr, nullptr, nullptr, H_, 256,
+                       WAh, WAh + (long)256*H_, 0);
+    g3(2, 1, Ch, Cl, H_, WAh, WAh + (long)256*H_, H_, 0,
+       H1, nullptr, nullptr, 256, 0, nullptr, nullptr,
+       sb1, nullptr, nullptr, H_, GF_RELU_OUT);
+    hipLaunchKernelGGL(gemm_kernel, dim3(NT_/BM, 2), dim3(256), 0, stream,
+                       H1, 256, sW2, TAGS_, logits, TAGS_, sb2, NT_, TAGS_, 256);
+
+    hipLaunchKernelGGL(crf_vit_kernel, dim3(B_, 2), dim3(512), 0, stream,
+                       logits, stgt, smask, crfs, crfe, crft, crfv, BPg, outf);
 
     hipLaunchKernelGGL(combine_kernel, dim3(1), dim3(64), 0, stream,
                        iloss, crfv, lv, outf);
```

Result: no change. 4.890 ms (-0.3%).
